# Performance work log

Measured on AMD Instinct MI355X. Metric: run time of the kernel, lower is better.

## Reference

```python
import jax, jax.numpy as jnp
import numpy as np
from jax import lax

B, L, K, OUT = 16384, 8192, 2, 128
L3 = L - 3 * (K - 1)  # 8189, length after 3 valid convs


def setup_inputs() -> dict:
    key = jax.random.key(0)
    ks = jax.random.split(key, 9)
    return {
        "x": jax.random.normal(ks[0], (B, 1, L), jnp.float32),
        "w1": jax.random.normal(ks[1], (1, 1, K), jnp.float32),
        "b1": jax.random.normal(ks[2], (1,), jnp.float32),
        "w2": jax.random.normal(ks[3], (1, 1, K), jnp.float32),
        "b2": jax.random.normal(ks[4], (1,), jnp.float32),
        "w3": jax.random.normal(ks[5], (1, 1, K), jnp.float32),
        "b3": jax.random.normal(ks[6], (1,), jnp.float32),
        "W": jax.random.normal(ks[7], (OUT, L3), jnp.float32) * 0.02,
        "b": jax.random.normal(ks[8], (OUT,), jnp.float32),
    }


def _conv1d(x, w, b):
    # x: [B, 1, L_in], w: [1, 1, K] (OIW), valid padding, stride 1
    y = lax.conv_general_dilated(x, w, window_strides=(1,), padding="VALID",
                                 dimension_numbers=("NCW", "OIW", "NCW"))
    return y + b[None, :, None]


def reference(x, w1, b1, w2, b2, w3, b3, W, b):
    h = jax.nn.relu(_conv1d(x, w1, b1))
    h = jax.nn.relu(_conv1d(h, w2, b2))
    h = jax.nn.relu(_conv1d(h, w3, b3))
    flat = h.reshape(h.shape[0], -1)          # [B, L3]
    return flat @ W.T + b                     # [B, OUT]
```

## Files before the change

### kernel.cpp

```cpp
#include <hip/hip_runtime.h>
#include <hip/hip_bf16.h>

typedef __attribute__((ext_vector_type(8))) short short8;
typedef __attribute__((ext_vector_type(8))) unsigned short ushort8;
typedef __attribute__((ext_vector_type(4))) float f32x4;

#define LIN  8192
#define L3V  8189
#define NOUT 128
#define KP   8192
#define BM   64
#define BK   64
#define NTH  64
#define PITCH (BK + 8)
#define NROW 16384

static __device__ __forceinline__ unsigned short f2bf(float f) {
    union { float f; unsigned u; } c; c.f = f;
    unsigned r = c.u + 0x7FFFu + ((c.u >> 16) & 1u);
    return (unsigned short)(r >> 16);
}

__global__ void wprep(const float* __restrict__ W, unsigned short* __restrict__ Wb) {
    int idx = blockIdx.x * 256 + threadIdx.x;
    int n = idx >> 13;
    int k = idx & (KP - 1);
    float v = (k < L3V) ? W[(size_t)n * L3V + k] : 0.0f;
    Wb[idx] = f2bf(v);
}

__global__ void reduce_out(const float* __restrict__ p,
                           const float* __restrict__ bias,
                           float* __restrict__ out) {
    const int idx = blockIdx.x * 256 + threadIdx.x;
    const float4 a = reinterpret_cast<const float4*>(p)[idx];
    const float4 c = reinterpret_cast<const float4*>(p)[idx + (NROW * NOUT / 4)];
    const float4 bb = *reinterpret_cast<const float4*>(bias + ((idx * 4) & (NOUT - 1)));
    float4 o;
    o.x = a.x + c.x + bb.x;
    o.y = a.y + c.y + bb.y;
    o.z = a.z + c.z + bb.z;
    o.w = a.w + c.w + bb.w;
    reinterpret_cast<float4*>(out)[idx] = o;
}

__global__ __launch_bounds__(512, 4) void fused(
    const float* __restrict__ x,
    const float* __restrict__ w1, const float* __restrict__ b1,
    const float* __restrict__ w2, const float* __restrict__ b2,
    const float* __restrict__ w3, const float* __restrict__ b3,
    const unsigned short* __restrict__ Wb,
    float* __restrict__ part)
{
    __shared__ unsigned short hA[2][BM * PITCH];
    __shared__ unsigned short wA[2][NOUT * PITCH];

    const int tid  = threadIdx.x;
    const int row0 = blockIdx.x * BM;
    const int kh   = blockIdx.y;
    const int tb   = kh * NTH;

    const float w10 = w1[0], w11 = w1[1], cb1 = b1[0];
    const float w20 = w2[0], w21 = w2[1], cb2 = b2[0];
    const float w30 = w3[0], w31 = w3[1], cb3 = b3[0];

    const int srow = tid >> 3;
    const int scol = (tid & 7) * 8;
    const float* xrow = x + (size_t)(row0 + srow) * LIN;

    const int wn = tid >> 2;
    const int wq = tid & 3;
    const unsigned short* wrow = Wb + (size_t)wn * KP + wq * 16;

    const int lane = tid & 63;
    const int wid  = tid >> 6;
    const int wr   = wid >> 1;
    const int wc   = wid & 1;
    const int l15  = lane & 15;
    const int koff = (lane >> 4) * 8;
    const int arow_off = (wr * 16 + l15) * PITCH + koff;

    f32x4 acc[4];
    #pragma unroll
    for (int f = 0; f < 4; ++f) acc[f] = (f32x4){0.f, 0.f, 0.f, 0.f};

    float   xv[12];
    ushort8 wv[2];

    auto stage_load = [&](int t) {
        const int gk = (tb + t) * BK + scol;
        if (gk + 12 <= LIN) {
            #pragma unroll
            for (int q = 0; q < 3; ++q) {
                const float4 v = *reinterpret_cast<const float4*>(xrow + gk + q * 4);
                xv[q*4+0] = v.x; xv[q*4+1] = v.y; xv[q*4+2] = v.z; xv[q*4+3] = v.w;
            }
        } else {
            #pragma unroll
            for (int q = 0; q < 2; ++q) {
                const float4 v = *reinterpret_cast<const float4*>(xrow + gk + q * 4);
                xv[q*4+0] = v.x; xv[q*4+1] = v.y; xv[q*4+2] = v.z; xv[q*4+3] = v.w;
            }
            xv[8] = 0.f; xv[9] = 0.f; xv[10] = 0.f; xv[11] = 0.f;
        }
        const ushort8* wsrc = reinterpret_cast<const ushort8*>(wrow + (tb + t) * BK);
        wv[0] = wsrc[0];
        wv[1] = wsrc[1];
    };

    auto stage_store = [&](int t, int s) {
        const int gk = (tb + t) * BK + scol;
        float h1[10];
        #pragma unroll
        for (int j = 0; j < 10; ++j)
            h1[j] = fmaxf(fmaf(w10, xv[j], fmaf(w11, xv[j+1], cb1)), 0.0f);
        float h2[9];
        #pragma unroll
        for (int j = 0; j < 9; ++j)
            h2[j] = fmaxf(fmaf(w20, h1[j], fmaf(w21, h1[j+1], cb2)), 0.0f);
        ushort8 hp;
        #pragma unroll
        for (int j = 0; j < 8; ++j) {
            float h3 = fmaxf(fmaf(w30, h2[j], fmaf(w31, h2[j+1], cb3)), 0.0f);
            hp[j] = (gk + j < L3V) ? f2bf(h3) : (unsigned short)0;
        }
        *reinterpret_cast<ushort8*>(&hA[s][srow * PITCH + scol]) = hp;
        ushort8* wdst = reinterpret_cast<ushort8*>(&wA[s][wn * PITCH + wq * 16]);
        wdst[0] = wv[0];
        wdst[1] = wv[1];
    };

    auto mfma_tile = [&](int s) {
        const unsigned short* hB = hA[s];
        const unsigned short* wB = wA[s];
        #pragma unroll
        for (int kk = 0; kk < BK; kk += 32) {
            const short8 af = *reinterpret_cast<const short8*>(&hB[arow_off + kk]);
            #pragma unroll
            for (int f = 0; f < 4; ++f) {
                const int bn = wc * 64 + f * 16 + l15;
                const short8 bf = *reinterpret_cast<const short8*>(&wB[bn * PITCH + kk + koff]);
                acc[f] = __builtin_amdgcn_mfma_f32_16x16x32_bf16(af, bf, acc[f], 0, 0, 0);
            }
        }
    };

    stage_load(0);
    stage_store(0, 0);
    stage_load(1);
    __syncthreads();

    int sel = 0;
    #pragma unroll 1
    for (int t = 0; t < NTH; ++t) {
        mfma_tile(sel);
        if (t + 1 < NTH) stage_store(t + 1, sel ^ 1);
        if (t + 2 < NTH) stage_load(t + 2);
        __syncthreads();
        sel ^= 1;
    }

    float* pbase = part + (size_t)kh * NROW * NOUT;
    #pragma unroll
    for (int f = 0; f < 4; ++f) {
        const int col = wc * 64 + f * 16 + l15;
        #pragma unroll
        for (int j = 0; j < 4; ++j) {
            const int grow = row0 + wr * 16 + (lane >> 4) * 4 + j;
            pbase[(size_t)grow * NOUT + col] = acc[f][j];
        }
    }
}

extern "C" void kernel_launch(void* const* d_in, const int* in_sizes, int n_in,
                              void* d_out, int out_size, void* d_ws, size_t ws_size,
                              hipStream_t stream) {
    const float* x  = (const float*)d_in[0];
    const float* w1 = (const float*)d_in[1];
    const float* b1 = (const float*)d_in[2];
    const float* w2 = (const float*)d_in[3];
    const float* b2 = (const float*)d_in[4];
    const float* w3 = (const float*)d_in[5];
    const float* b3 = (const float*)d_in[6];
    const float* W  = (const float*)d_in[7];
    const float* b  = (const float*)d_in[8];
    float* out = (float*)d_out;

    unsigned short* Wb   = (unsigned short*)d_ws;
    float*          part = (float*)((char*)d_ws + (2u << 20));

    wprep<<<dim3((NOUT * KP) / 256), dim3(256), 0, stream>>>(W, Wb);
    fused<<<dim3(NROW / BM, 2), dim3(512), 0, stream>>>(
        x, w1, b1, w2, b2, w3, b3, Wb, part);
    reduce_out<<<dim3(NROW * NOUT / 4 / 256), dim3(256), 0, stream>>>(part, b, out);
}
```

Before: 146.0 us.

## Enlarge fused tile to 128x128 with two M-fragments per wave

Doubles the row tile and K tile of the fused conv+GEMM kernel, so each wave computes two 16-row MFMA fragments that share each loaded W fragment. Each thread now computes 32 conv outputs per stage instead of 8, which cuts the redundant halo recomputation and the W reload per output row. The aim is to halve the number of W tile loads from global memory and LDS per output row. The cost is higher register and LDS use, so the launch bound drops to 2 blocks per CU and occupancy falls.

```diff
diff --git a/kernel.cpp b/kernel.cpp
--- a/kernel.cpp
+++ b/kernel.cpp
@@ -9,9 +9,9 @@
 #define L3V  8189
 #define NOUT 128
 #define KP   8192
-#define BM   64
-#define BK   64
-#define NTH  64
+#define BM   128
+#define BK   128
+#define NTH  32
 #define PITCH (BK + 8)
 #define NROW 16384
 
@@ -44,7 +44,7 @@
     reinterpret_cast<float4*>(out)[idx] = o;
 }
 
-__global__ __launch_bounds__(512, 4) void fused(
+__global__ __launch_bounds__(512, 2) void fused(
     const float* __restrict__ x,
     const float* __restrict__ w1, const float* __restrict__ b1,
     const float* __restrict__ w2, const float* __restrict__ b2,
@@ -64,13 +64,13 @@
     const float w20 = w2[0], w21 = w2[1], cb2 = b2[0];
     const float w30 = w3[0], w31 = w3[1], cb3 = b3[0];
 
-    const int srow = tid >> 3;
-    const int scol = (tid & 7) * 8;
+    const int srow = tid >> 2;
+    const int scol = (tid & 3) * 32;
     const float* xrow = x + (size_t)(row0 + srow) * LIN;
 
     const int wn = tid >> 2;
     const int wq = tid & 3;
-    const unsigned short* wrow = Wb + (size_t)wn * KP + wq * 16;
+    const unsigned short* wrow = Wb + (size_t)wn * KP + wq * 32;
 
     const int lane = tid & 63;
     const int wid  = tid >> 6;
@@ -78,69 +78,76 @@
     const int wc   = wid & 1;
     const int l15  = lane & 15;
     const int koff = (lane >> 4) * 8;
-    const int arow_off = (wr * 16 + l15) * PITCH + koff;
-
-    f32x4 acc[4];
+    const int arow0 = (wr * 32 + l15) * PITCH + koff;
+    const int arow1 = arow0 + 16 * PITCH;
+
+    f32x4 acc[2][4];
     #pragma unroll
-    for (int f = 0; f < 4; ++f) acc[f] = (f32x4){0.f, 0.f, 0.f, 0.f};
-
-    float   xv[12];
-    ushort8 wv[2];
+    for (int m = 0; m < 2; ++m)
+        #pragma unroll
+        for (int f = 0; f < 4; ++f) acc[m][f] = (f32x4){0.f, 0.f, 0.f, 0.f};
+
+    float   xv[36];
+    ushort8 wv[4];
 
     auto stage_load = [&](int t) {
         const int gk = (tb + t) * BK + scol;
-        if (gk + 12 <= LIN) {
-            #pragma unroll
-            for (int q = 0; q < 3; ++q) {
+        if (gk + 36 <= LIN) {
+            #pragma unroll
+            for (int q = 0; q < 9; ++q) {
                 const float4 v = *reinterpret_cast<const float4*>(xrow + gk + q * 4);
                 xv[q*4+0] = v.x; xv[q*4+1] = v.y; xv[q*4+2] = v.z; xv[q*4+3] = v.w;
             }
         } else {
             #pragma unroll
-            for (int q = 0; q < 2; ++q) {
+            for (int q = 0; q < 8; ++q) {
                 const float4 v = *reinterpret_cast<const float4*>(xrow + gk + q * 4);
                 xv[q*4+0] = v.x; xv[q*4+1] = v.y; xv[q*4+2] = v.z; xv[q*4+3] = v.w;
             }
-            xv[8] = 0.f; xv[9] = 0.f; xv[10] = 0.f; xv[11] = 0.f;
+            xv[32] = 0.f; xv[33] = 0.f; xv[34] = 0.f; xv[35] = 0.f;
         }
         const ushort8* wsrc = reinterpret_cast<const ushort8*>(wrow + (tb + t) * BK);
-        wv[0] = wsrc[0];
-        wv[1] = wsrc[1];
+        #pragma unroll
+        for (int i = 0; i < 4; ++i) wv[i] = wsrc[i];
     };
 
     auto stage_store = [&](int t, int s) {
         const int gk = (tb + t) * BK + scol;
-        float h1[10];
-        #pragma unroll
-        for (int j = 0; j < 10; ++j)
+        float h1[35];
+        #pragma unroll
+        for (int j = 0; j < 35; ++j)
             h1[j] = fmaxf(fmaf(w10, xv[j], fmaf(w11, xv[j+1], cb1)), 0.0f);
-        float h2[9];
-        #pragma unroll
-        for (int j = 0; j < 9; ++j)
+        float h2[34];
+        #pragma unroll
+        for (int j = 0; j < 34; ++j)
             h2[j] = fmaxf(fmaf(w20, h1[j], fmaf(w21, h1[j+1], cb2)), 0.0f);
-        ushort8 hp;
-        #pragma unroll
-        for (int j = 0; j < 8; ++j) {
+        ushort8 hp[4];
+        #pragma unroll
+        for (int j = 0; j < 32; ++j) {
             float h3 = fmaxf(fmaf(w30, h2[j], fmaf(w31, h2[j+1], cb3)), 0.0f);
-            hp[j] = (gk + j < L3V) ? f2bf(h3) : (unsigned short)0;
-        }
-        *reinterpret_cast<ushort8*>(&hA[s][srow * PITCH + scol]) = hp;
-        ushort8* wdst = reinterpret_cast<ushort8*>(&wA[s][wn * PITCH + wq * 16]);
-        wdst[0] = wv[0];
-        wdst[1] = wv[1];
+            hp[j >> 3][j & 7] = (gk + j < L3V) ? f2bf(h3) : (unsigned short)0;
+        }
+        ushort8* hd = reinterpret_cast<ushort8*>(&hA[s][srow * PITCH + scol]);
+        #pragma unroll
+        for (int i = 0; i < 4; ++i) hd[i] = hp[i];
+        ushort8* wdst = reinterpret_cast<ushort8*>(&wA[s][wn * PITCH + wq * 32]);
+        #pragma unroll
+        for (int i = 0; i < 4; ++i) wdst[i] = wv[i];
     };
 
     auto mfma_tile = [&](int s) {
         const unsigned short* hB = hA[s];
         const unsigned short* wB = wA[s];
         #pragma unroll
-        for (int kk = 0; kk < BK; kk += 32) {
-            const short8 af = *reinterpret_cast<const short8*>(&hB[arow_off + kk]);
+        for (int ks = 0; ks < 4; ++ks) {
+            const short8 af0 = *reinterpret_cast<const short8*>(&hB[arow0 + ks * 32]);
+            const short8 af1 = *reinterpret_cast<const short8*>(&hB[arow1 + ks * 32]);
             #pragma unroll
             for (int f = 0; f < 4; ++f) {
                 const int bn = wc * 64 + f * 16 + l15;
-                const short8 bf = *reinterpret_cast<const short8*>(&wB[bn * PITCH + kk + koff]);
-                acc[f] = __builtin_amdgcn_mfma_f32_16x16x32_bf16(af, bf, acc[f], 0, 0, 0);
+                const short8 bf = *reinterpret_cast<const short8*>(&wB[bn * PITCH + ks * 32 + koff]);
+                acc[0][f] = __builtin_amdgcn_mfma_f32_16x16x32_bf16(af0, bf, acc[0][f], 0, 0, 0);
+                acc[1][f] = __builtin_amdgcn_mfma_f32_16x16x32_bf16(af1, bf, acc[1][f], 0, 0, 0);
             }
         }
     };
@@ -162,12 +169,15 @@
 
     float* pbase = part + (size_t)kh * NROW * NOUT;
     #pragma unroll
-    for (int f = 0; f < 4; ++f) {
-        const int col = wc * 64 + f * 16 + l15;
-        #pragma unroll
-        for (int j = 0; j < 4; ++j) {
-            const int grow = row0 + wr * 16 + (lane >> 4) * 4 + j;
-            pbase[(size_t)grow * NOUT + col] = acc[f][j];
+    for (int m = 0; m < 2; ++m) {
+        #pragma unroll
+        for (int f = 0; f < 4; ++f) {
+            const int col = wc * 64 + f * 16 + l15;
+            #pragma unroll
+            for (int j = 0; j < 4; ++j) {
+                const int grow = row0 + wr * 32 + m * 16 + (lane >> 4) * 4 + j;
+                pbase[(size_t)grow * NOUT + col] = acc[m][f][j];
+            }
         }
     }
 }
```

New measurement: 192.6 us. +31.9%, slower.
